# Kernel tuning notes

Measured on AMD Instinct MI355X. Metric: run time of the kernel, lower is better.

Reference implementation:

```python
import jax, jax.numpy as jnp
import numpy as np

N = 100000          # primal nodes
ND = 1600000        # dual (line-graph) nodes = primal edges
E = 1600000         # primal edges
ED = 3200000        # dual edges
F_IN, HEADS, HID, NCLS, F_DUAL = 512, 8, 8, 16, 4
NEG_SLOPE = 0.2     # PyG GATConv default negative_slope


def _with_self_loops(edge_index, n):
    loops = jnp.arange(n, dtype=edge_index.dtype)
    src = jnp.concatenate([edge_index[0], loops])
    dst = jnp.concatenate([edge_index[1], loops])
    return src, dst


def _gat(x, src, dst, W, a_src, a_dst, b, heads, out_ch, concat, n):
    # PyG GATConv (eval mode, attention dropout off), self loops already added.
    h = (x @ W).reshape(n, heads, out_ch)                      # [n, H, C]
    alpha_s = jnp.einsum('nhc,hc->nh', h, a_src)               # [n, H]
    alpha_d = jnp.einsum('nhc,hc->nh', h, a_dst)
    e = jax.nn.leaky_relu(alpha_s[src] + alpha_d[dst], NEG_SLOPE)  # [E, H]
    m = jax.ops.segment_max(e, dst, num_segments=n)            # per-dst max
    m = jnp.where(jnp.isfinite(m), m, 0.0)
    ex = jnp.exp(e - m[dst])
    denom = jax.ops.segment_sum(ex, dst, num_segments=n)
    alpha = ex / (denom[dst] + 1e-16)                          # segment softmax
    out = jax.ops.segment_sum(h[src] * alpha[:, :, None], dst, num_segments=n)
    out = out.reshape(n, heads * out_ch) if concat else out.mean(axis=1)
    return out + b


def _gcn(x, src, dst, W, b, n):
    h = x @ W
    deg = jax.ops.segment_sum(jnp.ones_like(dst, dtype=h.dtype), dst, num_segments=n)
    dinv = jax.lax.rsqrt(jnp.maximum(deg, 1.0))  # deg >= 1 because of self loops
    norm = dinv[src] * dinv[dst]
    out = jax.ops.segment_sum(norm[:, None] * h[src], dst, num_segments=n)
    return out + b


def setup_inputs():
    key = jax.random.key(0)
    ks = jax.random.split(key, 14)
    s = 0.1
    return {
        'x': jax.random.normal(ks[0], (N, F_IN), jnp.float32),
        'edge_index': jax.random.randint(ks[1], (2, E), 0, N, jnp.int32),
        'dual_x': jax.random.normal(ks[2], (ND, F_DUAL), jnp.float32),
        'dual_edge_index': jax.random.randint(ks[3], (2, ED), 0, ND, jnp.int32),
        # GATConv 1: in=512 -> heads=8, out=8, concat
        'W1': jax.random.normal(ks[4], (F_IN, HEADS * HID), jnp.float32) * s,
        'att_src1': jax.random.normal(ks[5], (HEADS, HID), jnp.float32) * s,
        'att_dst1': jax.random.normal(ks[6], (HEADS, HID), jnp.float32) * s,
        'b1': jnp.zeros((HEADS * HID,), jnp.float32),
        # GATConv 2: in=64 -> heads=1, out=16, mean
        'W2': jax.random.normal(ks[7], (HEADS * HID, 1 * NCLS), jnp.float32) * s,
        'att_src2': jax.random.normal(ks[8], (1, NCLS), jnp.float32) * s,
        'att_dst2': jax.random.normal(ks[9], (1, NCLS), jnp.float32) * s,
        'b2': jnp.zeros((NCLS,), jnp.float32),
        # dual GCNConv stack: 4 -> 8 -> 16
        'Wg1': jax.random.normal(ks[10], (F_DUAL, HID), jnp.float32) * s,
        'bg1': jnp.zeros((HID,), jnp.float32),
        'Wg2': jax.random.normal(ks[11], (HID, NCLS), jnp.float32) * s,
        'bg2': jnp.zeros((NCLS,), jnp.float32),
    }


def reference(x, edge_index, dual_x, dual_edge_index,
              W1, att_src1, att_dst1, b1,
              W2, att_src2, att_dst2, b2,
              Wg1, bg1, Wg2, bg2):
    # dual (line-graph) GCN branch
    ds, dd = _with_self_loops(dual_edge_index, ND)
    Q1 = jax.nn.relu(_gcn(dual_x, ds, dd, Wg1, bg1, ND))
    Q = _gcn(Q1, ds, dd, Wg2, bg2, ND)
    # primal GAT branch (dropout = identity in eval mode)
    s_, d_ = _with_self_loops(edge_index, N)
    h = jax.nn.elu(_gat(x, s_, d_, W1, att_src1, att_dst1, b1, HEADS, HID, True, N))
    out = _gat(h, s_, d_, W2, att_src2, att_dst2, b2, 1, NCLS, False, N)
    return (out, Q)
```

## Files before the change

kernel.cpp:

```cpp
#include <hip/hip_runtime.h>
#include <math.h>

#define NP    100000
#define EP    1600000
#define NDU   1600000
#define EDU   3200000
#define FIN   512
#define NHEAD 8
#define HIDC  8
#define NCLS  16
#define NEGS  0.2f
#define TPB   256

static __device__ __forceinline__ float lrelu(float x){ return x > 0.f ? x : NEGS*x; }


#define BKT_MAX 256
#define BCHUNK  2048

__global__ void k_bhist(const int* __restrict__ dst, int* __restrict__ bcnt,
                        int n, int shift){
  __shared__ int cnt[BKT_MAX];
  for(int i=threadIdx.x;i<BKT_MAX;i+=TPB) cnt[i]=0;
  __syncthreads();
  int base = blockIdx.x*BCHUNK;
  #pragma unroll
  for(int i=0;i<8;i++){
    int e = base + i*TPB + threadIdx.x;
    if(e<n) atomicAdd(&cnt[dst[e]>>shift],1);
  }
  __syncthreads();
  for(int i=threadIdx.x;i<BKT_MAX;i+=TPB) if(cnt[i]) atomicAdd(bcnt+i, cnt[i]);
}

__global__ void k_bscan(int* __restrict__ bcnt, int nb){
  __shared__ int lds[BKT_MAX];
  for(int i=threadIdx.x;i<nb;i+=TPB) lds[i]=bcnt[i];
  __syncthreads();
  if(threadIdx.x==0){ int s=0; for(int i=0;i<nb;i++){ int v=lds[i]; lds[i]=s; s+=v; } }
  __syncthreads();
  for(int i=threadIdx.x;i<nb;i+=TPB) bcnt[i]=lds[i];
}

__global__ __launch_bounds__(TPB) void k_bscat(const int* __restrict__ src,
                                               const int* __restrict__ dst,
                                               int* __restrict__ btail,
                                               int2* __restrict__ pairs,
                                               int n, int shift){
  __shared__ int cnt[BKT_MAX];
  __shared__ int bbase[BKT_MAX];
  for(int i=threadIdx.x;i<BKT_MAX;i+=TPB) cnt[i]=0;
  __syncthreads();
  int base = blockIdx.x*BCHUNK;
  int sv[8], dv[8], rv[8];
  #pragma unroll
  for(int i=0;i<8;i++){
    int e = base + i*TPB + threadIdx.x;
    if(e<n){ sv[i]=src[e]; dv[i]=dst[e]; rv[i]=atomicAdd(&cnt[dv[i]>>shift],1); }
    else rv[i]=-1;
  }
  __syncthreads();
  for(int i=threadIdx.x;i<BKT_MAX;i+=TPB){
    int c = cnt[i];
    bbase[i] = c ? atomicAdd(btail+i, c) : 0;
  }
  __syncthreads();
  #pragma unroll
  for(int i=0;i<8;i++){
    if(rv[i]>=0){
      int b = dv[i]>>shift;
      pairs[bbase[b]+rv[i]] = make_int2(sv[i], dv[i]);
    }
  }
}

__global__ __launch_bounds__(TPB) void k_csr(const int2* __restrict__ pairs,
                                             const int* __restrict__ btail,
                                             int* __restrict__ offs,
                                             float* __restrict__ dinv,
                                             int* __restrict__ col,
                                             int nnodes, int shift){
  extern __shared__ int ldeg[];
  __shared__ int ttmp[TPB];
  const int b    = blockIdx.x;
  const int tid  = threadIdx.x;
  const int ebeg = b ? btail[b-1] : 0;
  const int eend = btail[b];
  const int node0 = b << shift;
  const int W     = 1 << shift;
  const int PW    = W / TPB;

  for(int i=tid;i<W;i+=TPB) ldeg[i]=0;
  __syncthreads();
  for(int e=ebeg+tid; e<eend; e+=TPB)
    atomicAdd(&ldeg[pairs[e].y - node0], 1);
  __syncthreads();

  const int base = tid*PW;
  int s = 0;
  for(int i=0;i<PW;i++) s += ldeg[base+i];
  ttmp[tid] = s; __syncthreads();
  for(int off=1; off<TPB; off<<=1){
    int t = (tid>=off)? ttmp[tid-off] : 0;
    __syncthreads(); ttmp[tid] += t; __syncthreads();
  }
  int run = ttmp[tid] - s;

  for(int i=0;i<PW;i++){
    int d  = base + i;
    int g  = node0 + d;
    int dg = ldeg[d];
    if(g < nnodes){
      offs[g] = ebeg + run + dg;
      dinv[g] = rsqrtf((float)dg + 1.0f);
    }
    ldeg[d] = ebeg + run;
    run += dg;
  }
  __syncthreads();

  for(int e=ebeg+tid; e<eend; e+=TPB){
    int2 p = pairs[e];
    int pos = atomicAdd(&ldeg[p.y - node0], 1);
    col[pos] = p.x;
  }
}


__global__ void k_pscale(const float* __restrict__ dx, const float* __restrict__ dinv,
                         float4* __restrict__ PX){
  int n = blockIdx.x*TPB + threadIdx.x;
  if(n >= NDU) return;
  float4 v = *(const float4*)(dx + (size_t)n*4);
  float s = dinv[n];
  PX[n] = make_float4(v.x*s, v.y*s, v.z*s, v.w*s);
}

__global__ __launch_bounds__(TPB) void k_dual1(const float* __restrict__ PX,
                                               const float* __restrict__ Wg1,
                                               const float* __restrict__ bg1,
                                               const float* __restrict__ dinv,
                                               const int* __restrict__ offs,
                                               const int* __restrict__ col,
                                               float* __restrict__ P2){
  int t = blockIdx.x*TPB + threadIdx.x;
  if(t >= NDU*4) return;
  int d = t >> 2, c = t & 3;
  int beg = d ? offs[d-1] : 0;
  int end = offs[d];
  float acc = PX[d*4 + c];
  for(int j=beg; j<end; j++) acc += PX[col[j]*4 + c];
  float v0 = __shfl(acc, 0, 4), v1 = __shfl(acc, 1, 4);
  float v2 = __shfl(acc, 2, 4), v3 = __shfl(acc, 3, 4);
  float di = dinv[d];
  int ch = 2*c;
  float z0 = di*(v0*Wg1[ch]   + v1*Wg1[8+ch]   + v2*Wg1[16+ch]   + v3*Wg1[24+ch])   + bg1[ch];
  float z1 = di*(v0*Wg1[ch+1] + v1*Wg1[8+ch+1] + v2*Wg1[16+ch+1] + v3*Wg1[24+ch+1]) + bg1[ch+1];
  z0 = z0 > 0.f ? z0 : 0.f;
  z1 = z1 > 0.f ? z1 : 0.f;
  *(float2*)(P2 + (size_t)d*8 + ch) = make_float2(di*z0, di*z1);
}

__global__ __launch_bounds__(TPB) void k_dual2(const float* __restrict__ P2,
                                               const float* __restrict__ Wg2,
                                               const float* __restrict__ bg2,
                                               const float* __restrict__ dinv,
                                               const int* __restrict__ offs,
                                               const int* __restrict__ col,
                                               float* __restrict__ Qo){
  int t = blockIdx.x*TPB + threadIdx.x;
  if(t >= NDU*8) return;
  int d = t >> 3, c = t & 7;
  int beg = d ? offs[d-1] : 0;
  int end = offs[d];
  float acc = P2[d*8 + c];
  for(int j=beg; j<end; j++) acc += P2[col[j]*8 + c];
  float v[8];
  #pragma unroll
  for(int k=0;k<8;k++) v[k] = __shfl(acc, k, 8);
  float di = dinv[d];
  int ch = 2*c;
  float z0 = 0.f, z1 = 0.f;
  #pragma unroll
  for(int k=0;k<8;k++){
    z0 += v[k]*Wg2[k*16 + ch];
    z1 += v[k]*Wg2[k*16 + ch + 1];
  }
  *(float2*)(Qo + (size_t)d*16 + ch) = make_float2(di*z0 + bg2[ch], di*z1 + bg2[ch+1]);
}


#define GBM 128
#define GBK 32
__global__ __launch_bounds__(TPB) void k_gemm1(const float* __restrict__ x,
                                               const float* __restrict__ W,
                                               float* __restrict__ H){
  __shared__ float xs[GBK][GBM+4];
  __shared__ float ws[GBK][64];
  const int tx = threadIdx.x;
  const int r0 = blockIdx.x*GBM;
  const int cg = tx & 15;
  const int rg = tx >> 4;

  float acc[8][4];
  #pragma unroll
  for(int i=0;i<8;i++)
    #pragma unroll
    for(int j=0;j<4;j++) acc[i][j] = 0.f;

  const int xrow = tx >> 3;
  const int xkc  = (tx & 7) * 4;
  const int wk = tx >> 4;
  const int wc = (tx & 15) * 4;

  for(int k0=0; k0<FIN; k0+=GBK){
    #pragma unroll
    for(int q=0;q<4;q++){
      int r  = xrow + q*32;
      int gr = r0 + r;
      float4 v = (gr < NP) ? *(const float4*)(x + (size_t)gr*FIN + k0 + xkc)
                           : make_float4(0.f,0.f,0.f,0.f);
      xs[xkc+0][r] = v.x; xs[xkc+1][r] = v.y;
      xs[xkc+2][r] = v.z; xs[xkc+3][r] = v.w;
    }
    #pragma unroll
    for(int q=0;q<2;q++){
      int k = wk + q*16;
      *(float4*)(&ws[k][wc]) = *(const float4*)(W + (size_t)(k0+k)*64 + wc);
    }
    __syncthreads();
    #pragma unroll 8
    for(int kk=0;kk<GBK;kk++){
      const float4 a0 = *(const float4*)(&xs[kk][rg*8]);
      const float4 a1 = *(const float4*)(&xs[kk][rg*8+4]);
      const float4 b  = *(const float4*)(&ws[kk][cg*4]);
      const float av[8] = {a0.x,a0.y,a0.z,a0.w,a1.x,a1.y,a1.z,a1.w};
      const float bv[4] = {b.x,b.y,b.z,b.w};
      #pragma unroll
      for(int i=0;i<8;i++)
        #pragma unroll
        for(int j=0;j<4;j++)
          acc[i][j] += av[i]*bv[j];
    }
    __syncthreads();
  }
  #pragma unroll
  for(int i=0;i<8;i++){
    int gr = r0 + rg*8 + i;
    if(gr < NP)
      *(float4*)(H + (size_t)gr*64 + cg*4) =
          make_float4(acc[i][0],acc[i][1],acc[i][2],acc[i][3]);
  }
}

__global__ void k_alpha(const float* __restrict__ H, const float* __restrict__ aw_s,
                        const float* __restrict__ aw_d,
                        float* __restrict__ als, float* __restrict__ ald){
  int i = blockIdx.x*TPB + threadIdx.x;
  if(i >= NP*NHEAD) return;
  int n = i >> 3, h = i & 7;
  const float* hp = H + n*64 + h*8;
  float s = 0.f, d = 0.f;
  #pragma unroll
  for(int c=0;c<8;c++){ float v = hp[c]; s += v*aw_s[h*8+c]; d += v*aw_d[h*8+c]; }
  als[i] = s; ald[i] = d;
}

__global__ __launch_bounds__(TPB) void k_agg1(const int* __restrict__ offs,
                                              const int* __restrict__ col,
                                              const float* __restrict__ als,
                                              const float* __restrict__ ald,
                                              const float* __restrict__ H,
                                              const float* __restrict__ b1,
                                              float* __restrict__ O){
  int d = (blockIdx.x*TPB + threadIdx.x) >> 6;
  int lane = threadIdx.x & 63;
  int hc = lane >> 3;
  int beg = d ? offs[d-1] : 0;
  int end = offs[d];
  float aldc = ald[d*8 + hc];
  float den0=0.f, den1=0.f, den2=0.f, den3=0.f;
  float acc0=0.f, acc1=0.f, acc2=0.f, acc3=0.f;
  int j = beg;
  for(; j+4<=end; j+=4){
    int s0=col[j], s1=col[j+1], s2=col[j+2], s3=col[j+3];
    float a0=als[s0*8+hc], a1=als[s1*8+hc], a2=als[s2*8+hc], a3=als[s3*8+hc];
    float h0=H[s0*64+lane], h1=H[s1*64+lane], h2=H[s2*64+lane], h3=H[s3*64+lane];
    float w0=__expf(lrelu(a0+aldc)); den0+=w0; acc0+=w0*h0;
    float w1=__expf(lrelu(a1+aldc)); den1+=w1; acc1+=w1*h1;
    float w2=__expf(lrelu(a2+aldc)); den2+=w2; acc2+=w2*h2;
    float w3=__expf(lrelu(a3+aldc)); den3+=w3; acc3+=w3*h3;
  }
  for(; j<end; j++){
    int s = col[j];
    float w = __expf(lrelu(als[s*8 + hc] + aldc));
    den0 += w;
    acc0 += w * H[s*64 + lane];
  }
  float ws = __expf(lrelu(als[d*8 + hc] + aldc));
  float den = ((den0+den1)+(den2+den3)) + ws;
  float acc = ((acc0+acc1)+(acc2+acc3)) + ws * H[d*64 + lane];
  float v = acc / (den + 1e-16f) + b1[lane];
  O[d*64 + lane] = v > 0.f ? v : expm1f(v);
}

__global__ void k_g(const float* __restrict__ O, const float* __restrict__ W2,
                    const float* __restrict__ asw, const float* __restrict__ adw,
                    float* __restrict__ G, float* __restrict__ as2, float* __restrict__ ad2){
  __shared__ float w2s[64*NCLS];
  for(int i=threadIdx.x; i<64*NCLS; i+=TPB) w2s[i] = W2[i];
  __syncthreads();
  int n = blockIdx.x*TPB + threadIdx.x;
  if(n >= NP) return;
  float g[16];
  #pragma unroll
  for(int c=0;c<16;c++) g[c] = 0.f;
  const float* op = O + n*64;
  #pragma unroll
  for(int k4=0;k4<64;k4+=4){
    float4 v = *(const float4*)(op + k4);
    #pragma unroll
    for(int c=0;c<16;c++){
      g[c] += v.x*w2s[(k4+0)*16+c] + v.y*w2s[(k4+1)*16+c]
            + v.z*w2s[(k4+2)*16+c] + v.w*w2s[(k4+3)*16+c];
    }
  }
  float s=0.f, t=0.f;
  #pragma unroll
  for(int c=0;c<16;c++){ s += g[c]*asw[c]; t += g[c]*adw[c]; }
  #pragma unroll
  for(int c4=0;c4<16;c4+=4)
    *(float4*)(G + n*16 + c4) = make_float4(g[c4],g[c4+1],g[c4+2],g[c4+3]);
  as2[n] = s; ad2[n] = t;
}

__global__ __launch_bounds__(TPB) void k_agg2(const int* __restrict__ offs,
                                              const int* __restrict__ col,
                                              const float* __restrict__ as2,
                                              const float* __restrict__ ad2,
                                              const float* __restrict__ G,
                                              const float* __restrict__ b2,
                                              float* __restrict__ out){
  int d = (blockIdx.x*TPB + threadIdx.x) >> 6;
  int lane = threadIdx.x & 63;
  int c = lane & 15, slot = lane >> 4;
  int beg = d ? offs[d-1] : 0;
  int end = offs[d];
  float ad2d = ad2[d];
  float den0=0.f, den1=0.f, acc0=0.f, acc1=0.f;
  for(int j0=beg; j0<end; j0+=8){
    int ja = j0 + slot;
    int jb = ja + 4;
    if(ja < end){
      int s = col[ja];
      float w = __expf(lrelu(as2[s] + ad2d));
      den0 += w; acc0 += w * G[s*16 + c];
    }
    if(jb < end){
      int s = col[jb];
      float w = __expf(lrelu(as2[s] + ad2d));
      den1 += w; acc1 += w * G[s*16 + c];
    }
  }
  float acc = acc0 + acc1, den = den0 + den1;
  acc += __shfl_xor(acc, 16);
  acc += __shfl_xor(acc, 32);
  den += __shfl_xor(den, 16);
  den += __shfl_xor(den, 32);
  float ws = __expf(lrelu(as2[d] + ad2d));
  den += ws;
  acc += ws * G[d*16 + c];
  if(lane < 16) out[d*16 + c] = acc / (den + 1e-16f) + b2[c];
}


extern "C" void kernel_launch(void* const* d_in, const int* in_sizes, int n_in,
                              void* d_out, int out_size, void* d_ws, size_t ws_size,
                              hipStream_t stream){
  const float* x    = (const float*)d_in[0];
  const int*   ei   = (const int*)  d_in[1];
  const float* dx   = (const float*)d_in[2];
  const int*   dei  = (const int*)  d_in[3];
  const float* W1   = (const float*)d_in[4];
  const float* aw1s = (const float*)d_in[5];
  const float* aw1d = (const float*)d_in[6];
  const float* b1   = (const float*)d_in[7];
  const float* W2   = (const float*)d_in[8];
  const float* aw2s = (const float*)d_in[9];
  const float* aw2d = (const float*)d_in[10];
  const float* b2   = (const float*)d_in[11];
  const float* Wg1  = (const float*)d_in[12];
  const float* bg1  = (const float*)d_in[13];
  const float* Wg2  = (const float*)d_in[14];
  const float* bg2  = (const float*)d_in[15];

  float* out = (float*)d_out;
  float* Qo  = out + NP*NCLS;

  float* R     = (float*)d_ws;
  float* dinvD = R + 25600000;
  int*   offsD = (int*)(dinvD + 1600000);
  int*   colD  = offsD + 1600000;
  int*   bkt   = colD + 3200000;

  int2*   pairsD = (int2*)R;
  float4* PX   = (float4*)R;
  float*  P2   = R + 6400000;
  float* H1   = R;
  float* O1   = R + 6400000;
  float* G    = R + 12800000;
  float* als  = R + 14400000;
  float* ald  = R + 15200000;
  float* as2  = R + 16000000;
  float* ad2  = R + 16100000;
  float* dinvP= R + 16200000;
  int*   offsP= (int*)(R + 16300000);
  int*   colP = offsP + 100000;
  int2*  pairsP = (int2*)(R + 19200000);

  const int* dsrc = dei;
  const int* ddst = dei + EDU;
  const int* esrc = ei;
  const int* edst = ei + EP;

  const int SH_D = 13, NB_D = ((NDU - 1) >> SH_D) + 1;
  const int SH_P = 9,  NB_P = ((NP  - 1) >> SH_P) + 1;

  hipMemsetAsync(bkt, 0, BKT_MAX*sizeof(int), stream);
  k_bhist<<<(EDU+BCHUNK-1)/BCHUNK, TPB, 0, stream>>>(ddst, bkt, EDU, SH_D);
  k_bscan<<<1, TPB, 0, stream>>>(bkt, NB_D);
  k_bscat<<<(EDU+BCHUNK-1)/BCHUNK, TPB, 0, stream>>>(dsrc, ddst, bkt, pairsD, EDU, SH_D);
  k_csr  <<<NB_D, TPB, (1<<SH_D)*sizeof(int), stream>>>(pairsD, bkt, offsD, dinvD, colD, NDU, SH_D);

  k_pscale<<<(NDU+TPB-1)/TPB, TPB, 0, stream>>>(dx, dinvD, PX);
  k_dual1 <<<NDU*4/TPB, TPB, 0, stream>>>((const float*)PX, Wg1, bg1, dinvD, offsD, colD, P2);
  k_dual2 <<<NDU*8/TPB, TPB, 0, stream>>>(P2, Wg2, bg2, dinvD, offsD, colD, Qo);

  hipMemsetAsync(bkt, 0, BKT_MAX*sizeof(int), stream);
  k_bhist<<<(EP+BCHUNK-1)/BCHUNK, TPB, 0, stream>>>(edst, bkt, EP, SH_P);
  k_bscan<<<1, TPB, 0, stream>>>(bkt, NB_P);
  k_bscat<<<(EP+BCHUNK-1)/BCHUNK, TPB, 0, stream>>>(esrc, edst, bkt, pairsP, EP, SH_P);
  k_csr  <<<NB_P, TPB, (1<<SH_P)*sizeof(int), stream>>>(pairsP, bkt, offsP, dinvP, colP, NP, SH_P);

  k_gemm1<<<(NP+GBM-1)/GBM, TPB, 0, stream>>>(x, W1, H1);
  k_alpha<<<NP*NHEAD/TPB, TPB, 0, stream>>>(H1, aw1s, aw1d, als, ald);
  k_agg1 <<<NP/4, TPB, 0, stream>>>(offsP, colP, als, ald, H1, b1, O1);
  k_g    <<<(NP+TPB-1)/TPB, TPB, 0, stream>>>(O1, W2, aw2s, aw2d, G, as2, ad2);
  k_agg2 <<<NP/4, TPB, 0, stream>>>(offsP, colP, as2, ad2, G, b2, out);
}
```

Baseline: 984.6 us.

## Double-buffer GEMM1 shared tiles and use 512 threads per block

The x@W1 GEMM now double-buffers the x and W tiles in shared memory, prefetching the next K-slice into registers while computing the current one, so only one barrier is needed per step. The block grows to 512 threads, each computing a 4x4 output tile instead of 8x4, which adds parallelism and cuts per-thread register use. The trade-off is less arithmetic per shared-memory load and twice the LDS per block, which may limit how many blocks fit per CU. The GEMM streams about 200 MB of x, so the gain depends on hiding memory latency better.

```diff
diff --git a/kernel.cpp b/kernel.cpp
--- a/kernel.cpp
+++ b/kernel.cpp
@@ -192,61 +192,77 @@
 
 #define GBM 128
 #define GBK 32
-__global__ __launch_bounds__(TPB) void k_gemm1(const float* __restrict__ x,
-                                               const float* __restrict__ W,
-                                               float* __restrict__ H){
-  __shared__ float xs[GBK][GBM+4];
-  __shared__ float ws[GBK][64];
+#define GT  512
+__global__ __launch_bounds__(GT) void k_gemm1(const float* __restrict__ x,
+                                              const float* __restrict__ W,
+                                              float* __restrict__ H){
+  __shared__ float xs[2][GBK][GBM+4];
+  __shared__ float ws[2][GBK][68];
   const int tx = threadIdx.x;
   const int r0 = blockIdx.x*GBM;
   const int cg = tx & 15;
   const int rg = tx >> 4;
 
-  float acc[8][4];
-  #pragma unroll
-  for(int i=0;i<8;i++)
+  float acc[4][4];
+  #pragma unroll
+  for(int i=0;i<4;i++)
     #pragma unroll
     for(int j=0;j<4;j++) acc[i][j] = 0.f;
 
   const int xrow = tx >> 3;
-  const int xkc  = (tx & 7) * 4;
+  const int xkc  = (tx & 7)*4;
   const int wk = tx >> 4;
-  const int wc = (tx & 15) * 4;
-
+  const int wc = (tx & 15)*4;
+
+  float4 xv0, xv1, wv;
+  {
+    int gr0 = r0 + xrow, gr1 = gr0 + 64;
+    xv0 = (gr0<NP)? *(const float4*)(x + (size_t)gr0*FIN + xkc) : make_float4(0,0,0,0);
+    xv1 = (gr1<NP)? *(const float4*)(x + (size_t)gr1*FIN + xkc) : make_float4(0,0,0,0);
+    wv  = *(const float4*)(W + (size_t)wk*64 + wc);
+    int r = xrow;
+    xs[0][xkc+0][r]=xv0.x; xs[0][xkc+1][r]=xv0.y; xs[0][xkc+2][r]=xv0.z; xs[0][xkc+3][r]=xv0.w;
+    r += 64;
+    xs[0][xkc+0][r]=xv1.x; xs[0][xkc+1][r]=xv1.y; xs[0][xkc+2][r]=xv1.z; xs[0][xkc+3][r]=xv1.w;
+    *(float4*)(&ws[0][wk][wc]) = wv;
+  }
+  __syncthreads();
+
+  int cur = 0;
   for(int k0=0; k0<FIN; k0+=GBK){
-    #pragma unroll
-    for(int q=0;q<4;q++){
-      int r  = xrow + q*32;
-      int gr = r0 + r;
-      float4 v = (gr < NP) ? *(const float4*)(x + (size_t)gr*FIN + k0 + xkc)
-                           : make_float4(0.f,0.f,0.f,0.f);
-      xs[xkc+0][r] = v.x; xs[xkc+1][r] = v.y;
-      xs[xkc+2][r] = v.z; xs[xkc+3][r] = v.w;
-    }
-    #pragma unroll
-    for(int q=0;q<2;q++){
-      int k = wk + q*16;
-      *(float4*)(&ws[k][wc]) = *(const float4*)(W + (size_t)(k0+k)*64 + wc);
-    }
-    __syncthreads();
+    int nk = k0 + GBK;
+    if(nk < FIN){
+      int gr0 = r0 + xrow, gr1 = gr0 + 64;
+      xv0 = (gr0<NP)? *(const float4*)(x + (size_t)gr0*FIN + nk + xkc) : make_float4(0,0,0,0);
+      xv1 = (gr1<NP)? *(const float4*)(x + (size_t)gr1*FIN + nk + xkc) : make_float4(0,0,0,0);
+      wv  = *(const float4*)(W + (size_t)(nk+wk)*64 + wc);
+    }
     #pragma unroll 8
     for(int kk=0;kk<GBK;kk++){
-      const float4 a0 = *(const float4*)(&xs[kk][rg*8]);
-      const float4 a1 = *(const float4*)(&xs[kk][rg*8+4]);
-      const float4 b  = *(const float4*)(&ws[kk][cg*4]);
-      const float av[8] = {a0.x,a0.y,a0.z,a0.w,a1.x,a1.y,a1.z,a1.w};
+      const float4 a = *(const float4*)(&xs[cur][kk][rg*4]);
+      const float4 b = *(const float4*)(&ws[cur][kk][cg*4]);
+      const float av[4] = {a.x,a.y,a.z,a.w};
       const float bv[4] = {b.x,b.y,b.z,b.w};
       #pragma unroll
-      for(int i=0;i<8;i++)
+      for(int i=0;i<4;i++)
         #pragma unroll
         for(int j=0;j<4;j++)
           acc[i][j] += av[i]*bv[j];
     }
-    __syncthreads();
-  }
-  #pragma unroll
-  for(int i=0;i<8;i++){
-    int gr = r0 + rg*8 + i;
+    if(nk < FIN){
+      int nxt = cur^1;
+      int r = xrow;
+      xs[nxt][xkc+0][r]=xv0.x; xs[nxt][xkc+1][r]=xv0.y; xs[nxt][xkc+2][r]=xv0.z; xs[nxt][xkc+3][r]=xv0.w;
+      r += 64;
+      xs[nxt][xkc+0][r]=xv1.x; xs[nxt][xkc+1][r]=xv1.y; xs[nxt][xkc+2][r]=xv1.z; xs[nxt][xkc+3][r]=xv1.w;
+      *(float4*)(&ws[nxt][wk][wc]) = wv;
+      __syncthreads();
+      cur = nxt;
+    }
+  }
+  #pragma unroll
+  for(int i=0;i<4;i++){
+    int gr = r0 + rg*4 + i;
     if(gr < NP)
       *(float4*)(H + (size_t)gr*64 + cg*4) =
           make_float4(acc[i][0],acc[i][1],acc[i][2],acc[i][3]);
@@ -442,7 +458,7 @@
   k_bscat<<<(EP+BCHUNK-1)/BCHUNK, TPB, 0, stream>>>(esrc, edst, bkt, pairsP, EP, SH_P);
   k_csr  <<<NB_P, TPB, (1<<SH_P)*sizeof(int), stream>>>(pairsP, bkt, offsP, dinvP, colP, NP, SH_P);
 
-  k_gemm1<<<(NP+GBM-1)/GBM, TPB, 0, stream>>>(x, W1, H1);
+  k_gemm1<<<(NP+GBM-1)/GBM, GT, 0, stream>>>(x, W1, H1);
   k_alpha<<<NP*NHEAD/TPB, TPB, 0, stream>>>(H1, aw1s, aw1d, als, ald);
   k_agg1 <<<NP/4, TPB, 0, stream>>>(offsP, colP, als, ald, H1, b1, O1);
   k_g    <<<(NP+TPB-1)/TPB, TPB, 0, stream>>>(O1, W2, aw2s, aw2d, G, as2, ad2);
```

Result: no change. 992.7 us (+0.8%).
